# Kernel optimization log

Measured on AMD Instinct MI355X. Metric: run time of the kernel, lower is better.

The kernel has to match this reference:

```python
import jax, jax.numpy as jnp
import numpy as np

N_WAY = 5
NKPTS = 17
EMBED = 512
N_SUPPORT = 25  # 5-way 5-shot
N_QUERY = 65536


def setup_inputs() -> dict:
    key = jax.random.key(0)
    ks = jax.random.split(key, 12)
    def lin(k, fan_in, fan_out):
        return jax.random.normal(k, (fan_in, fan_out), jnp.float32) / np.float32(np.sqrt(fan_in))
    return {
        'support_features': jax.random.normal(ks[0], (1, N_SUPPORT, EMBED), jnp.float32),
        'support_keypoints': jax.random.uniform(ks[1], (N_SUPPORT, NKPTS, 2), jnp.float32),
        'query_features': jax.random.normal(ks[2], (N_QUERY, EMBED), jnp.float32),
        'image_coords': jax.random.uniform(ks[3], (N_QUERY, 2), jnp.float32) * 512.0,
        'W1': lin(ks[4], EMBED, EMBED), 'b1': jnp.zeros((EMBED,), jnp.float32),
        'W2': lin(ks[5], EMBED, EMBED), 'b2': jnp.zeros((EMBED,), jnp.float32),
        'Wo1': lin(ks[6], EMBED, EMBED // 2), 'bo1': jnp.zeros((EMBED // 2,), jnp.float32),
        'Wo2': lin(ks[7], EMBED // 2, 2), 'bo2': jnp.zeros((2,), jnp.float32),
        'Wc1': lin(ks[8], EMBED, EMBED // 2), 'bc1': jnp.zeros((EMBED // 2,), jnp.float32),
        'Wc2': lin(ks[9], EMBED // 2, 1), 'bc2': jnp.zeros((1,), jnp.float32),
        'temperature': jnp.float32(1.0),
    }


def reference(support_features, support_keypoints, query_features, image_coords,
              W1, b1, W2, b2, Wo1, bo1, Wo2, bo2, Wc1, bc1, Wc2, bc2, temperature):
    eps = 1e-8
    nkpts = support_keypoints.shape[1]
    n_query = query_features.shape[0]
    D = query_features.shape[-1]

    # --- compute_prototypes (batch_size == 1; per-kpt prototype identical by construction) ---
    sf = support_features.reshape(-1, D)                      # [Ns, D]
    h = jnp.maximum(sf @ W1 + b1, 0.0) @ W2 + b2              # prototype_net MLP
    n_per = h.shape[0] // N_WAY
    proto_way = h.reshape(N_WAY, n_per, D).mean(axis=1)       # [n_way, D]
    prototypes = jnp.broadcast_to(proto_way[:, None, :], (N_WAY, nkpts, D))

    # --- compute_distances: 1 - cosine_sim, scaled by temperature ---
    qn = jnp.linalg.norm(query_features, axis=-1)             # [Nq]
    pn = jnp.linalg.norm(proto_way, axis=-1)                  # [n_way]
    sim = (query_features @ proto_way.T) / jnp.maximum(qn[:, None] * pn[None, :], eps)
    dist_way = (1.0 - sim) / temperature                      # [Nq, n_way]
    distances = jnp.broadcast_to(dist_way[:, :, None], (n_query, N_WAY, nkpts))

    # --- predict_keypoints ---
    # avg over kpts is a no-op (identical per kpt); argmin over ways
    class_predictions = jnp.argmin(dist_way, axis=1)          # [Nq] int
    # softmax over a single scalar == 1.0, so keypoints == offset broadcast over kpts
    offset = jnp.maximum(query_features @ Wo1 + bo1, 0.0) @ Wo2 + bo2   # [Nq, 2]
    conf = jax.nn.sigmoid(jnp.maximum(query_features @ Wc1 + bc1, 0.0) @ Wc2 + bc2)  # [Nq, 1]
    keypoints = jnp.broadcast_to(offset[:, None, :], (n_query, nkpts, 2))
    keypoints = jax.nn.sigmoid(keypoints) * image_coords[:, None, :]    # image_coords provided
    confidence = jnp.broadcast_to(conf, (n_query, nkpts))

    return keypoints, confidence, distances, class_predictions, prototypes
```

## Files before the change

kernel.cpp:

```cpp
#include <hip/hip_runtime.h>
#include <hip/hip_bf16.h>

#define NQ 65536
#define DIM 512
#define HID 256
#define NWAY 5
#define NKPTS 17

typedef short bf16x8 __attribute__((ext_vector_type(8)));
typedef float f32x4 __attribute__((ext_vector_type(4)));
typedef _Float16 half8 __attribute__((ext_vector_type(8)));

static __device__ __forceinline__ unsigned short f2bf(float f) {
    unsigned int x = __float_as_uint(f);
    unsigned int r = (x + 0x7fffu + ((x >> 16) & 1u)) >> 16;
    return (unsigned short)r;
}

static __device__ __forceinline__ void async16(void* l, const void* g) {
    __builtin_amdgcn_global_load_lds(
        (const __attribute__((address_space(1))) unsigned int*)g,
        (__attribute__((address_space(3))) unsigned int*)l, 16, 0, 0);
}

__global__ __launch_bounds__(256) void k_sup(const float* __restrict__ sf,
                                             const float* __restrict__ W1, const float* __restrict__ b1,
                                             float* __restrict__ ws_h1) {
    __shared__ float sfl[512];
    __shared__ float red[4][64];
    int bx = blockIdx.x;
    int s = bx >> 3, cb = bx & 7;
    int t = threadIdx.x;
    if (t < 128) ((float4*)sfl)[t] = ((const float4*)(sf + s * DIM))[t];
    __syncthreads();
    int c = cb * 64 + (t & 63);
    int qd = t >> 6;
    const float* Wp = W1 + (size_t)qd * 128 * DIM + c;
    float acc = 0.0f;
    #pragma unroll 4
    for (int kk = 0; kk < 128; kk++)
        acc += sfl[qd * 128 + kk] * Wp[(size_t)kk * DIM];
    red[qd][t & 63] = acc;
    __syncthreads();
    if (t < 64) {
        float h = red[0][t] + red[1][t] + red[2][t] + red[3][t] + b1[cb * 64 + t];
        ws_h1[s * DIM + cb * 64 + t] = fmaxf(h, 0.0f);
    }
}

__global__ __launch_bounds__(256) void k_mid2(const float* __restrict__ ws_h1,
                                              const float* __restrict__ W2, const float* __restrict__ b2,
                                              const float* __restrict__ Wo1, const float* __restrict__ Wc1,
                                              float* __restrict__ ws_proto, unsigned short* __restrict__ wb) {
    int bx = blockIdx.x;
    int t = threadIdx.x;
    if (bx < 40) {
        __shared__ float ml[512];
        __shared__ float red[4][64];
        int w = bx >> 3, cb = bx & 7;
        for (int i = t; i < 512; i += 256) {
            float sum = 0.0f;
            #pragma unroll
            for (int s5 = 0; s5 < 5; s5++) sum += ws_h1[(w * 5 + s5) * DIM + i];
            ml[i] = sum * 0.2f;
        }
        __syncthreads();
        int c = cb * 64 + (t & 63);
        int qd = t >> 6;
        const float* Wp = W2 + (size_t)qd * 128 * DIM + c;
        float acc = 0.0f;
        #pragma unroll 4
        for (int kk = 0; kk < 128; kk++)
            acc += ml[qd * 128 + kk] * Wp[(size_t)kk * DIM];
        red[qd][t & 63] = acc;
        __syncthreads();
        if (t < 64)
            ws_proto[w * DIM + cb * 64 + t] =
                red[0][t] + red[1][t] + red[2][t] + red[3][t] + b2[cb * 64 + t];
    } else {
        __shared__ unsigned short T[64][72];
        int tb = bx - 40;
        const float* src = (tb < 32) ? Wo1 : Wc1;
        int cofs = (tb < 32) ? 0 : 256;
        int tt = tb & 31;
        int kt = tt >> 2;
        int ct = tt & 3;
        int i = t >> 2;
        int qd = t & 3;
        const float* rp = src + (size_t)(kt * 64 + i) * HID + ct * 64 + qd * 16;
        #pragma unroll
        for (int v = 0; v < 4; v++) {
            float4 x = *(const float4*)(rp + v * 4);
            T[qd * 16 + v * 4 + 0][i] = f2bf(x.x);
            T[qd * 16 + v * 4 + 1][i] = f2bf(x.y);
            T[qd * 16 + v * 4 + 2][i] = f2bf(x.z);
            T[qd * 16 + v * 4 + 3][i] = f2bf(x.w);
        }
        __syncthreads();
        int j = t >> 2;
        int part = t & 3;
        uint4 o0 = *(const uint4*)&T[j][part * 16];
        uint4 o1 = *(const uint4*)&T[j][part * 16 + 8];
        unsigned short* dst = wb + (size_t)(cofs + ct * 64 + j) * DIM + kt * 64 + part * 16;
        *(uint4*)dst = o0;
        *(uint4*)(dst + 8) = o1;
    }
}

__global__ __launch_bounds__(512, 2) void k_fused2(const float* __restrict__ qf,
                                                   const unsigned short* __restrict__ wb,
                                                   const float* __restrict__ ws_proto,
                                                   const float* __restrict__ temp_p,
                                                   const float* __restrict__ bo1, const float* __restrict__ Wo2,
                                                   const float* __restrict__ bo2,
                                                   const float* __restrict__ bc1, const float* __restrict__ Wc2,
                                                   const float* __restrict__ bc2,
                                                   const float* __restrict__ ic,
                                                   float* __restrict__ out_kp, float* __restrict__ out_conf,
                                                   float* __restrict__ out_dist, float* __restrict__ out_class,
                                                   float* __restrict__ out_proto) {
    __shared__ __align__(16) char smem[94752];
    char* Abase = smem;
    char* Bbase = smem + 16384;
    float* s_proto = (float*)(smem + 81920);
    float* pn_lds = (float*)(smem + 92160);
    float* dlds = (float*)(smem + 92192);
    _Float16* hl = (_Float16*)smem;
    float* redf = (float*)(smem + 67584);

    int mb = blockIdx.x;
    int t = threadIdx.x;
    int wv = t >> 6, lane = t & 63;
    int wr = wv >> 2, wc = wv & 3;
    int r = lane & 15, hq = lane >> 4;

    for (int i = t; i < NWAY * DIM; i += 512) s_proto[i] = ws_proto[i];
    if (mb < NWAY * NKPTS && t < 128) {
        f32x4 v = *(const f32x4*)(ws_proto + (mb / NKPTS) * DIM + t * 4);
        *(f32x4*)(out_proto + (size_t)mb * DIM + t * 4) = v;
    }
    float invt = 1.0f / temp_p[0];

    int srow = lane >> 2;
    int sg = (lane & 3) ^ (srow & 3);
    const unsigned short* Bg = wb + ((size_t)wv * 64 + srow) * DIM + sg * 8;

    int am = t >> 2, akc = t & 3;
    const float* Ag = qf + ((size_t)mb * 128 + am) * DIM + akc * 8;
    int awoff = am * 64 + ((akc ^ (am & 3)) * 16);

    f32x4 acc[4][8];
    #pragma unroll
    for (int i2 = 0; i2 < 4; i2++)
        #pragma unroll
        for (int j2 = 0; j2 < 8; j2++) { f32x4 z = {0.0f, 0.0f, 0.0f, 0.0f}; acc[i2][j2] = z; }
    float ds[NWAY] = {0, 0, 0, 0, 0};
    float qq = 0.0f;

    float4 a0 = *(const float4*)(Ag);
    float4 a1 = *(const float4*)(Ag + 4);
    #pragma unroll
    for (int i = 0; i < 4; i++)
        async16(Bbase + wv * 4096 + i * 1024, Bg + (size_t)i * 16 * DIM);

    #pragma unroll 2
    for (int it = 0; it < 16; it++) {
        int par = it & 1;
        unsigned int p0 = f2bf(a0.x) | ((unsigned int)f2bf(a0.y) << 16);
        unsigned int p1 = f2bf(a0.z) | ((unsigned int)f2bf(a0.w) << 16);
        unsigned int p2 = f2bf(a1.x) | ((unsigned int)f2bf(a1.y) << 16);
        unsigned int p3 = f2bf(a1.z) | ((unsigned int)f2bf(a1.w) << 16);
        *(uint4*)(Abase + par * 8192 + awoff) = make_uint4(p0, p1, p2, p3);
        float av[8] = {a0.x, a0.y, a0.z, a0.w, a1.x, a1.y, a1.z, a1.w};
        int kb = it * 32 + akc * 8;
        #pragma unroll
        for (int w = 0; w < NWAY; w++) {
            f32x4 pv0 = *(const f32x4*)(s_proto + w * DIM + kb);
            f32x4 pv1 = *(const f32x4*)(s_proto + w * DIM + kb + 4);
            ds[w] += av[0] * pv0[0] + av[1] * pv0[1] + av[2] * pv0[2] + av[3] * pv0[3]
                   + av[4] * pv1[0] + av[5] * pv1[1] + av[6] * pv1[2] + av[7] * pv1[3];
        }
        #pragma unroll
        for (int j = 0; j < 8; j++) qq += av[j] * av[j];
        if (it < 15) {
            int ko = (it + 1) * 32;
            a0 = *(const float4*)(Ag + ko);
            a1 = *(const float4*)(Ag + ko + 4);
            #pragma unroll
            for (int i = 0; i < 4; i++)
                async16(Bbase + (par ^ 1) * 32768 + wv * 4096 + i * 1024,
                        Bg + (size_t)i * 16 * DIM + ko);
        }
        __syncthreads();
        const unsigned short* Ap = (const unsigned short*)(Abase + par * 8192);
        const unsigned short* Bp = (const unsigned short*)(Bbase + par * 32768);
        int sl = (hq ^ (r & 3)) * 8;
        bf16x8 af[4], bfr[8];
        #pragma unroll
        for (int mt = 0; mt < 4; mt++)
            af[mt] = *(const bf16x8*)(Ap + (wr * 64 + mt * 16 + r) * 32 + sl);
        #pragma unroll
        for (int nt = 0; nt < 8; nt++)
            bfr[nt] = *(const bf16x8*)(Bp + (wc * 128 + nt * 16 + r) * 32 + sl);
        #pragma unroll
        for (int mt = 0; mt < 4; mt++)
            #pragma unroll
            for (int nt = 0; nt < 8; nt++)
                acc[mt][nt] = __builtin_amdgcn_mfma_f32_16x16x32_bf16(af[mt], bfr[nt], acc[mt][nt], 0, 0, 0);
    }

    __syncthreads();

    if (wv < NWAY) {
        f32x4 a = *(const f32x4*)(s_proto + wv * DIM + lane * 8);
        f32x4 b = *(const f32x4*)(s_proto + wv * DIM + lane * 8 + 4);
        float ss = a[0]*a[0] + a[1]*a[1] + a[2]*a[2] + a[3]*a[3]
                 + b[0]*b[0] + b[1]*b[1] + b[2]*b[2] + b[3]*b[3];
        #pragma unroll
        for (int off = 32; off > 0; off >>= 1) ss += __shfl_xor(ss, off, 64);
        if (lane == 0) pn_lds[wv] = sqrtf(ss);
    }
    if (wc < 2) {
        #pragma unroll
        for (int nt = 0; nt < 8; nt++) {
            int cl = wc * 128 + nt * 16 + r;
            float bv = bo1[cl];
            #pragma unroll
            for (int mt = 0; mt < 4; mt++)
                #pragma unroll
                for (int rg = 0; rg < 4; rg++) {
                    int ml = wr * 64 + mt * 16 + hq * 4 + rg;
                    hl[ml * 264 + cl] = (_Float16)fmaxf(acc[mt][nt][rg] + bv, 0.0f);
                }
        }
    }
    __syncthreads();

    #pragma unroll
    for (int off = 1; off <= 2; off <<= 1) {
        #pragma unroll
        for (int w = 0; w < NWAY; w++) ds[w] += __shfl_xor(ds[w], off, 64);
        qq += __shfl_xor(qq, off, 64);
    }
    if (akc == 0) {
        float qn = sqrtf(qq);
        float mv = 1e30f; int ami = 0;
        #pragma unroll
        for (int w = 0; w < NWAY; w++) {
            float den = fmaxf(qn * pn_lds[w], 1e-8f);
            float d = (1.0f - ds[w] / den) * invt;
            dlds[am * 5 + w] = d;
            if (d < mv) { mv = d; ami = w; }
        }
        out_class[mb * 128 + am] = (float)ami;
    }
    {
        int q = t & 127, qt = t >> 7;
        float ox = 0.0f, oy = 0.0f;
        #pragma unroll 2
        for (int j0 = 0; j0 < 64; j0 += 8) {
            half8 hv = *(const half8*)(hl + q * 264 + qt * 64 + j0);
            #pragma unroll
            for (int j = 0; j < 8; j++) {
                float2 w2 = *(const float2*)(Wo2 + (qt * 64 + j0 + j) * 2);
                float hf = (float)hv[j];
                ox += hf * w2.x;
                oy += hf * w2.y;
            }
        }
        redf[(qt * 128 + q) * 2] = ox;
        redf[(qt * 128 + q) * 2 + 1] = oy;
    }
    __syncthreads();

    if (t < 128) {
        float sx = bo2[0], sy = bo2[1];
        #pragma unroll
        for (int k2 = 0; k2 < 4; k2++) {
            sx += redf[(k2 * 128 + t) * 2];
            sy += redf[(k2 * 128 + t) * 2 + 1];
        }
        size_t Q = (size_t)mb * 128 + t;
        float2 icv = *(const float2*)(ic + Q * 2);
        float gx = icv.x / (1.0f + __expf(-sx));
        float gy = icv.y / (1.0f + __expf(-sy));
        float2 g2 = make_float2(gx, gy);
        float2* dst = (float2*)(out_kp + Q * 34);
        #pragma unroll
        for (int k2 = 0; k2 < 17; k2++) dst[k2] = g2;
    }
    if (wc >= 2) {
        #pragma unroll
        for (int nt = 0; nt < 8; nt++) {
            int cl = (wc - 2) * 128 + nt * 16 + r;
            float bv = bc1[cl];
            #pragma unroll
            for (int mt = 0; mt < 4; mt++)
                #pragma unroll
                for (int rg = 0; rg < 4; rg++) {
                    int ml = wr * 64 + mt * 16 + hq * 4 + rg;
                    hl[ml * 264 + cl] = (_Float16)fmaxf(acc[mt][nt][rg] + bv, 0.0f);
                }
        }
    }
    for (int i = t; i < 128 * NWAY * NKPTS; i += 512) {
        int q2 = i / (NWAY * NKPTS);
        int rem = i - q2 * (NWAY * NKPTS);
        out_dist[(size_t)(mb * 128 + q2) * (NWAY * NKPTS) + rem] = dlds[q2 * 5 + rem / NKPTS];
    }
    __syncthreads();

    {
        int q = t & 127, qt = t >> 7;
        float cs = 0.0f;
        #pragma unroll 2
        for (int j0 = 0; j0 < 64; j0 += 8) {
            half8 hv = *(const half8*)(hl + q * 264 + qt * 64 + j0);
            #pragma unroll
            for (int j = 0; j < 8; j++)
                cs += (float)hv[j] * Wc2[qt * 64 + j0 + j];
        }
        redf[qt * 128 + q] = cs;
    }
    __syncthreads();
    if (t < 128) {
        float s = bc2[0] + redf[t] + redf[128 + t] + redf[256 + t] + redf[384 + t];
        float sg2 = 1.0f / (1.0f + __expf(-s));
        size_t Q = (size_t)mb * 128 + t;
        float* dst = out_conf + Q * 17;
        #pragma unroll
        for (int k2 = 0; k2 < 17; k2++) dst[k2] = sg2;
    }
}

extern "C" void kernel_launch(void* const* d_in, const int* in_sizes, int n_in,
                              void* d_out, int out_size, void* d_ws, size_t ws_size,
                              hipStream_t stream) {
    const float* sf = (const float*)d_in[0];
    const float* qf = (const float*)d_in[2];
    const float* ic = (const float*)d_in[3];
    const float* W1 = (const float*)d_in[4];
    const float* b1 = (const float*)d_in[5];
    const float* W2 = (const float*)d_in[6];
    const float* b2 = (const float*)d_in[7];
    const float* Wo1 = (const float*)d_in[8];
    const float* bo1 = (const float*)d_in[9];
    const float* Wo2 = (const float*)d_in[10];
    const float* bo2 = (const float*)d_in[11];
    const float* Wc1 = (const float*)d_in[12];
    const float* bc1 = (const float*)d_in[13];
    const float* Wc2 = (const float*)d_in[14];
    const float* bc2 = (const float*)d_in[15];
    const float* temp = (const float*)d_in[16];

    float* out = (float*)d_out;
    float* out_kp = out;
    float* out_conf = out + 2228224;
    float* out_dist = out + 3342336;
    float* out_class = out + 8912896;
    float* out_proto = out + 8978432;

    char* ws = (char*)d_ws;
    float* ws_h1 = (float*)ws;
    float* ws_proto = (float*)(ws + 51200);
    unsigned short* ws_wb = (unsigned short*)(ws + 65536);

    hipLaunchKernelGGL(k_sup, dim3(200), dim3(256), 0, stream, sf, W1, b1, ws_h1);
    hipLaunchKernelGGL(k_mid2, dim3(104), dim3(256), 0, stream, ws_h1, W2, b2, Wo1, Wc1, ws_proto, ws_wb);
    hipLaunchKernelGGL(k_fused2, dim3(512), dim3(512), 0, stream, qf, ws_wb, ws_proto, temp,
                       bo1, Wo2, bo2, bc1, Wc2, bc2, ic, out_kp, out_conf,
                       out_dist, out_class, out_proto);
}
```

Baseline: 319.1 us.

## Triple-buffer B tiles with prefetch distance two and raw barriers

```diff
diff --git a/kernel.cpp b/kernel.cpp
--- a/kernel.cpp
+++ b/kernel.cpp
@@ -107,24 +107,24 @@
     }
 }
 
-__global__ __launch_bounds__(512, 2) void k_fused2(const float* __restrict__ qf,
-                                                   const unsigned short* __restrict__ wb,
-                                                   const float* __restrict__ ws_proto,
-                                                   const float* __restrict__ temp_p,
-                                                   const float* __restrict__ bo1, const float* __restrict__ Wo2,
-                                                   const float* __restrict__ bo2,
-                                                   const float* __restrict__ bc1, const float* __restrict__ Wc2,
-                                                   const float* __restrict__ bc2,
-                                                   const float* __restrict__ ic,
-                                                   float* __restrict__ out_kp, float* __restrict__ out_conf,
-                                                   float* __restrict__ out_dist, float* __restrict__ out_class,
-                                                   float* __restrict__ out_proto) {
-    __shared__ __align__(16) char smem[94752];
+__global__ __launch_bounds__(512) void k_fused3(const float* __restrict__ qf,
+                                                const unsigned short* __restrict__ wb,
+                                                const float* __restrict__ ws_proto,
+                                                const float* __restrict__ temp_p,
+                                                const float* __restrict__ bo1, const float* __restrict__ Wo2,
+                                                const float* __restrict__ bo2,
+                                                const float* __restrict__ bc1, const float* __restrict__ Wc2,
+                                                const float* __restrict__ bc2,
+                                                const float* __restrict__ ic,
+                                                float* __restrict__ out_kp, float* __restrict__ out_conf,
+                                                float* __restrict__ out_dist, float* __restrict__ out_class,
+                                                float* __restrict__ out_proto) {
+    __shared__ __align__(16) char smem[127520];
     char* Abase = smem;
     char* Bbase = smem + 16384;
-    float* s_proto = (float*)(smem + 81920);
-    float* pn_lds = (float*)(smem + 92160);
-    float* dlds = (float*)(smem + 92192);
+    float* s_proto = (float*)(smem + 114688);
+    float* dlds = (float*)(smem + 124928);
+    float* pn_lds = (float*)(smem + 127488);
     _Float16* hl = (_Float16*)smem;
     float* redf = (float*)(smem + 67584);
 
@@ -140,15 +140,25 @@
         *(f32x4*)(out_proto + (size_t)mb * DIM + t * 4) = v;
     }
     float invt = 1.0f / temp_p[0];
-
+    __syncthreads();
+
+    if (wv < NWAY) {
+        f32x4 a = *(const f32x4*)(s_proto + wv * DIM + lane * 8);
+        f32x4 b = *(const f32x4*)(s_proto + wv * DIM + lane * 8 + 4);
+        float ss = a[0]*a[0] + a[1]*a[1] + a[2]*a[2] + a[3]*a[3]
+                 + b[0]*b[0] + b[1]*b[1] + b[2]*b[2] + b[3]*b[3];
+        #pragma unroll
+        for (int off = 32; off > 0; off >>= 1) ss += __shfl_xor(ss, off, 64);
+        if (lane == 0) pn_lds[wv] = sqrtf(ss);
+    }
+
+    int am = t >> 2, akc = t & 3;
+    const float* Ag = qf + ((size_t)mb * 128 + am) * DIM + akc * 8;
+    int awoff = am * 64 + ((akc ^ (am & 3)) * 16);
     int srow = lane >> 2;
     int sg = (lane & 3) ^ (srow & 3);
     const unsigned short* Bg = wb + ((size_t)wv * 64 + srow) * DIM + sg * 8;
 
-    int am = t >> 2, akc = t & 3;
-    const float* Ag = qf + ((size_t)mb * 128 + am) * DIM + akc * 8;
-    int awoff = am * 64 + ((akc ^ (am & 3)) * 16);
-
     f32x4 acc[4][8];
     #pragma unroll
     for (int i2 = 0; i2 < 4; i2++)
@@ -157,22 +167,25 @@
     float ds[NWAY] = {0, 0, 0, 0, 0};
     float qq = 0.0f;
 
-    float4 a0 = *(const float4*)(Ag);
-    float4 a1 = *(const float4*)(Ag + 4);
+    float4 aW0 = *(const float4*)(Ag);
+    float4 aW1 = *(const float4*)(Ag + 4);
+    float4 aN0 = *(const float4*)(Ag + 32);
+    float4 aN1 = *(const float4*)(Ag + 36);
     #pragma unroll
     for (int i = 0; i < 4; i++)
-        async16(Bbase + wv * 4096 + i * 1024, Bg + (size_t)i * 16 * DIM);
-
-    #pragma unroll 2
-    for (int it = 0; it < 16; it++) {
-        int par = it & 1;
-        unsigned int p0 = f2bf(a0.x) | ((unsigned int)f2bf(a0.y) << 16);
-        unsigned int p1 = f2bf(a0.z) | ((unsigned int)f2bf(a0.w) << 16);
-        unsigned int p2 = f2bf(a1.x) | ((unsigned int)f2bf(a1.y) << 16);
-        unsigned int p3 = f2bf(a1.z) | ((unsigned int)f2bf(a1.w) << 16);
-        *(uint4*)(Abase + par * 8192 + awoff) = make_uint4(p0, p1, p2, p3);
-        float av[8] = {a0.x, a0.y, a0.z, a0.w, a1.x, a1.y, a1.z, a1.w};
-        int kb = it * 32 + akc * 8;
+        async16(Bbase + (wv * 4 + i) * 1024, Bg + (size_t)i * 16 * DIM);
+    #pragma unroll
+    for (int i = 0; i < 4; i++)
+        async16(Bbase + 32768 + (wv * 4 + i) * 1024, Bg + (size_t)i * 16 * DIM + 32);
+
+    {
+        unsigned int p0 = f2bf(aW0.x) | ((unsigned int)f2bf(aW0.y) << 16);
+        unsigned int p1 = f2bf(aW0.z) | ((unsigned int)f2bf(aW0.w) << 16);
+        unsigned int p2 = f2bf(aW1.x) | ((unsigned int)f2bf(aW1.y) << 16);
+        unsigned int p3 = f2bf(aW1.z) | ((unsigned int)f2bf(aW1.w) << 16);
+        *(uint4*)(Abase + awoff) = make_uint4(p0, p1, p2, p3);
+        float av[8] = {aW0.x, aW0.y, aW0.z, aW0.w, aW1.x, aW1.y, aW1.z, aW1.w};
+        int kb = akc * 8;
         #pragma unroll
         for (int w = 0; w < NWAY; w++) {
             f32x4 pv0 = *(const f32x4*)(s_proto + w * DIM + kb);
@@ -182,18 +195,48 @@
         }
         #pragma unroll
         for (int j = 0; j < 8; j++) qq += av[j] * av[j];
+    }
+    aW0 = aN0; aW1 = aN1;
+
+    asm volatile("s_waitcnt lgkmcnt(0) vmcnt(4)" ::: "memory");
+    __builtin_amdgcn_s_barrier();
+    __builtin_amdgcn_sched_barrier(0);
+
+    #pragma unroll 2
+    for (int it = 0; it < 16; it++) {
+        int apar = it & 1;
+        int bpar = it % 3;
+        float4 aL0, aL1;
+        if (it < 14) {
+            int ko = (it + 2) * 32;
+            aL0 = *(const float4*)(Ag + ko);
+            aL1 = *(const float4*)(Ag + ko + 4);
+            int bp2 = (it + 2) % 3;
+            #pragma unroll
+            for (int i = 0; i < 4; i++)
+                async16(Bbase + bp2 * 32768 + (wv * 4 + i) * 1024,
+                        Bg + (size_t)i * 16 * DIM + ko);
+        }
         if (it < 15) {
-            int ko = (it + 1) * 32;
-            a0 = *(const float4*)(Ag + ko);
-            a1 = *(const float4*)(Ag + ko + 4);
-            #pragma unroll
-            for (int i = 0; i < 4; i++)
-                async16(Bbase + (par ^ 1) * 32768 + wv * 4096 + i * 1024,
-                        Bg + (size_t)i * 16 * DIM + ko);
-        }
-        __syncthreads();
-        const unsigned short* Ap = (const unsigned short*)(Abase + par * 8192);
-        const unsigned short* Bp = (const unsigned short*)(Bbase + par * 32768);
+            unsigned int p0 = f2bf(aW0.x) | ((unsigned int)f2bf(aW0.y) << 16);
+            unsigned int p1 = f2bf(aW0.z) | ((unsigned int)f2bf(aW0.w) << 16);
+            unsigned int p2 = f2bf(aW1.x) | ((unsigned int)f2bf(aW1.y) << 16);
+            unsigned int p3 = f2bf(aW1.z) | ((unsigned int)f2bf(aW1.w) << 16);
+            *(uint4*)(Abase + (apar ^ 1) * 8192 + awoff) = make_uint4(p0, p1, p2, p3);
+            float av[8] = {aW0.x, aW0.y, aW0.z, aW0.w, aW1.x, aW1.y, aW1.z, aW1.w};
+            int kb = (it + 1) * 32 + akc * 8;
+            #pragma unroll
+            for (int w = 0; w < NWAY; w++) {
+                f32x4 pv0 = *(const f32x4*)(s_proto + w * DIM + kb);
+                f32x4 pv1 = *(const f32x4*)(s_proto + w * DIM + kb + 4);
+                ds[w] += av[0] * pv0[0] + av[1] * pv0[1] + av[2] * pv0[2] + av[3] * pv0[3]
+                       + av[4] * pv1[0] + av[5] * pv1[1] + av[6] * pv1[2] + av[7] * pv1[3];
+            }
+            #pragma unroll
+            for (int j = 0; j < 8; j++) qq += av[j] * av[j];
+        }
+        const unsigned short* Ap = (const unsigned short*)(Abase + apar * 8192);
+        const unsigned short* Bp = (const unsigned short*)(Bbase + bpar * 32768);
         int sl = (hq ^ (r & 3)) * 8;
         bf16x8 af[4], bfr[8];
         #pragma unroll
@@ -207,19 +250,16 @@
             #pragma unroll
             for (int nt = 0; nt < 8; nt++)
                 acc[mt][nt] = __builtin_amdgcn_mfma_f32_16x16x32_bf16(af[mt], bfr[nt], acc[mt][nt], 0, 0, 0);
-    }
-
-    __syncthreads();
-
-    if (wv < NWAY) {
-        f32x4 a = *(const f32x4*)(s_proto + wv * DIM + lane * 8);
-        f32x4 b = *(const f32x4*)(s_proto + wv * DIM + lane * 8 + 4);
-        float ss = a[0]*a[0] + a[1]*a[1] + a[2]*a[2] + a[3]*a[3]
-                 + b[0]*b[0] + b[1]*b[1] + b[2]*b[2] + b[3]*b[3];
-        #pragma unroll
-        for (int off = 32; off > 0; off >>= 1) ss += __shfl_xor(ss, off, 64);
-        if (lane == 0) pn_lds[wv] = sqrtf(ss);
-    }
+        if (it < 15) {
+            if (it < 14) { asm volatile("s_waitcnt lgkmcnt(0) vmcnt(6)" ::: "memory"); }
+            else         { asm volatile("s_waitcnt lgkmcnt(0) vmcnt(0)" ::: "memory"); }
+            __builtin_amdgcn_s_barrier();
+            __builtin_amdgcn_sched_barrier(0);
+        }
+        if (it < 14) { aW0 = aL0; aW1 = aL1; }
+    }
+    __syncthreads();
+
     if (wc < 2) {
         #pragma unroll
         for (int nt = 0; nt < 8; nt++) {
@@ -367,7 +407,7 @@
 
     hipLaunchKernelGGL(k_sup, dim3(200), dim3(256), 0, stream, sf, W1, b1, ws_h1);
     hipLaunchKernelGGL(k_mid2, dim3(104), dim3(256), 0, stream, ws_h1, W2, b2, Wo1, Wc1, ws_proto, ws_wb);
-    hipLaunchKernelGGL(k_fused2, dim3(512), dim3(512), 0, stream, qf, ws_wb, ws_proto, temp,
+    hipLaunchKernelGGL(k_fused3, dim3(512), dim3(512), 0, stream, qf, ws_wb, ws_proto, temp,
                        bo1, Wo2, bo2, bc1, Wc2, bc2, ic, out_kp, out_conf,
                        out_dist, out_class, out_proto);
 }
```

Result: no change. 318.2 us (-0.3%).
